# Kernel optimization log

Measured on AMD Instinct MI355X. Metric: run time of the kernel, lower is better.

Reference implementation:

```python
import jax, jax.numpy as jnp
import numpy as np

EMBED_DIM = 512
Q_DIM = 64
V_DIM = 64
WINDOW_SIZE = 128
B, N = 2, 4096


def setup_inputs() -> dict:
    key = jax.random.key(0)
    ks = jax.random.split(key, 7)
    s = 1.0 / np.sqrt(EMBED_DIM)
    u = lambda k, shape: jax.random.uniform(k, shape, jnp.float32, -s, s)
    return {
        "x": jax.random.normal(ks[0], (B, N, EMBED_DIM), jnp.float32),
        "Wq": u(ks[1], (EMBED_DIM, Q_DIM)),
        "bq": u(ks[2], (Q_DIM,)),
        "Wk": u(ks[3], (EMBED_DIM, Q_DIM)),
        "bk": u(ks[4], (Q_DIM,)),
        "Wv": u(ks[5], (EMBED_DIM, V_DIM)),
        "bv": u(ks[6], (V_DIM,)),
    }


def reference(x, Wq, bq, Wk, bk, Wv, bv):
    b, n, _ = x.shape
    w = WINDOW_SIZE // 2
    Q = x @ Wq + bq  # (b, n, Qd)
    K = x @ Wk + bk  # (b, n, Qd)
    V = x @ Wv + bv  # (b, n, Vd)

    diags = jnp.arange(-w, w + 1)            # (nd,) offsets di
    nd = diags.shape[0]
    # Gather K[i + di] via padded K; invalid positions masked to 0 afterwards.
    Kpad = jnp.pad(K, ((0, 0), (w, w), (0, 0)))
    j = jnp.arange(n)[:, None] + diags[None, :]          # (n, nd) = i + di
    Kg = Kpad[:, j + w, :]                               # (b, n, nd, Qd)
    scores = jnp.einsum('bnd,bnod->bno', Q, Kg)          # (b, n, nd)
    valid = (j >= 0) & (j < n)
    scores = jnp.where(valid[None], scores, 0.0)

    # Faithful to original: diagonal dot products are scattered into the FIRST
    # nd columns of a dense (b, n, n) matrix (rest zeros), softmax over the
    # full n columns, then dense matmul with V.
    columns = jnp.zeros((b, n, n), dtype=x.dtype).at[:, :, :nd].set(scores)
    attn = jax.nn.softmax(columns, axis=2)               # (b, n, n)
    return attn @ V                                      # (b, n, Vd)
```

## Files before the change

### kernel.cpp

```cpp
#include <hip/hip_runtime.h>

typedef _Float16 half8 __attribute__((ext_vector_type(8)));
typedef float f32x4 __attribute__((ext_vector_type(4)));

#define NN 4096
#define NE 512
#define HD 64
#define KROWS 4288
#define KOFF  64
#define WSCALE (1.0f / 256.0f)

__device__ __forceinline__ void f16_split(float f, _Float16& hi, _Float16& lo) {
    hi = (_Float16)f;
    lo = (_Float16)(f - (float)hi);
}

#define MFMA16(a, b, c) __builtin_amdgcn_mfma_f32_16x16x32_f16((a), (b), (c), 0, 0, 0)

__global__ __launch_bounds__(256) void wprep_kernel(
    const float* __restrict__ Wq, const float* __restrict__ Wk,
    const float* __restrict__ Wv,
    _Float16* __restrict__ Wf, _Float16* __restrict__ Khi,
    _Float16* __restrict__ Vf, float* __restrict__ Vs)
{
    const int gtid = blockIdx.x * 256 + threadIdx.x;
    const int L = gtid & 63;
    {
        const int nt = (gtid >> 6) % 12;
        const int kt = gtid / 768;
        const int n = nt * 16 + (L & 15);
        const int kbase = kt * 32 + (L >> 4) * 8;
        const float* src; int col;
        if (n < 64)       { src = Wq; col = n; }
        else if (n < 128) { src = Wk; col = n - 64; }
        else              { src = Wv; col = n - 128; }
        half8 sh;
#pragma unroll
        for (int j = 0; j < 8; ++j)
            sh[j] = (_Float16)src[(size_t)(kbase + j) * HD + col];
        *(half8*)(Wf + (size_t)gtid * 8) = sh;
    }
    if (gtid < 6144) {
        const int p = gtid >> 3, o = gtid & 7;
        const int b = p / 192, q = p - b * 192;
        const size_t row = (size_t)b * KROWS + (q < 64 ? q : 4096 + q);
        const half8 z = {0, 0, 0, 0, 0, 0, 0, 0};
        *(half8*)(Khi + row * HD + o * 8) = z;
    }
    if (gtid < 3200) {
        const int rem = gtid % 1600;
        const int jt = rem / 320;
        const int nt = (rem / 64) % 5;
        half8 sh = {0, 0, 0, 0, 0, 0, 0, 0};
        if (nt == 4 && (L & 15) == 0) {
#pragma unroll
            for (int jj = 0; jj < 8; ++jj) {
                const int j = jt * 32 + (L >> 4) * 8 + jj;
                if (j < 129) sh[jj] = (_Float16)1.0f;
            }
        }
        *(half8*)(Vf + (size_t)gtid * 8) = sh;
    }
    if (gtid < 128) Vs[gtid] = 0.f;
}

__global__ __launch_bounds__(1024, 4) void proj_kernel(
    const float* __restrict__ x, const _Float16* __restrict__ Wf,
    const float* __restrict__ bq, const float* __restrict__ bk,
    const float* __restrict__ bv,
    _Float16* __restrict__ Qhi, _Float16* __restrict__ Qlo,
    _Float16* __restrict__ Khi, _Float16* __restrict__ Vf,
    float* __restrict__ Vs)
{
    __shared__ float parts[2][4][3][64][4];
    __shared__ float V_lds[32][68];
    const int tid = threadIdx.x;
    const int L = tid & 63;
    const int w = tid >> 6;
    const int m = L & 15, kg = L >> 4;
    const int blk = blockIdx.x;
    const int b = blk >> 7;
    const int mt = w >> 3;
    const int t3 = (w >> 1) & 3;
    const int h = w & 1;
    const int r0 = blk * 32;
    const int rr = r0 + mt * 16;

    const float* xp = x + (size_t)(rr + m) * NE + h * 256 + kg * 8;
    const _Float16* wfb = Wf + ((size_t)(h * 8) * 12 + t3 * 3) * 512 + L * 8;

    f32x4 acc[3];
#pragma unroll
    for (int t = 0; t < 3; ++t) acc[t] = (f32x4){0.f, 0.f, 0.f, 0.f};

#pragma unroll
    for (int kt = 0; kt < 8; ++kt) {
        const float4 x0 = *(const float4*)(xp + kt * 32);
        const float4 x1 = *(const float4*)(xp + kt * 32 + 4);
        const float xv[8] = {x0.x, x0.y, x0.z, x0.w, x1.x, x1.y, x1.z, x1.w};
        half8 ahi, alo;
#pragma unroll
        for (int j = 0; j < 8; ++j) {
            _Float16 hh, ll; f16_split(xv[j], hh, ll);
            ahi[j] = hh; alo[j] = ll;
        }
#pragma unroll
        for (int t = 0; t < 3; ++t) {
            const half8 wv = *(const half8*)(wfb + (size_t)kt * 6144 + t * 512);
            acc[t] = MFMA16(ahi, wv, acc[t]);
            acc[t] = MFMA16(alo, wv, acc[t]);
        }
    }

    if (h == 1) {
#pragma unroll
        for (int t = 0; t < 3; ++t)
            *(f32x4*)(&parts[mt][t3][t][L][0]) = acc[t];
    }
    __syncthreads();

    if (h == 0) {
#pragma unroll
        for (int t = 0; t < 3; ++t) {
            const f32x4 p = *(const f32x4*)(&parts[mt][t3][t][L][0]);
            acc[t] += p;
            const int nt = t3 * 3 + t;
            const int cgc = nt * 16 + m;
            const float bias = (cgc < 64) ? bq[cgc]
                             : (cgc < 128) ? bk[cgc - 64] : bv[cgc - 128];
#pragma unroll
            for (int r = 0; r < 4; ++r) {
                const int gr = rr + kg * 4 + r;
                const float val = acc[t][r] + bias;
                if (cgc < 64) {
                    _Float16 hh, ll; f16_split(val, hh, ll);
                    Qhi[(size_t)gr * HD + cgc] = hh;
                    Qlo[(size_t)gr * HD + cgc] = ll;
                } else if (cgc < 128) {
                    const int d = cgc - 64, n = gr & 4095;
                    Khi[((size_t)b * KROWS + KOFF + n) * HD + d] = (_Float16)val;
                } else {
                    V_lds[mt * 16 + kg * 4 + r][cgc - 128] = val;
                }
            }
        }
    }
    __syncthreads();

    if (tid < 64) {
        float s = 0.f;
#pragma unroll
        for (int r = 0; r < 32; ++r) s += V_lds[r][tid];
        atomicAdd(&Vs[b * HD + tid], s);
    }

    {
        const int local = blk & 127;
        if (local < 4 && w < 4) {
            const int jt = local;
            const int nt = w;
            half8 sh;
#pragma unroll
            for (int jj = 0; jj < 8; ++jj)
                sh[jj] = (_Float16)V_lds[kg * 8 + jj][nt * 16 + m];
            const size_t fo = ((size_t)((b * 25 + jt * 5 + nt) * 64 + L)) * 8;
            *(half8*)(Vf + fo) = sh;
        } else if (local == 4 && w < 4 && kg == 0) {
            const int nt = w;
            half8 sh = {0, 0, 0, 0, 0, 0, 0, 0};
            sh[0] = (_Float16)V_lds[0][nt * 16 + m];
            const size_t fo = ((size_t)((b * 25 + 4 * 5 + nt) * 64 + L)) * 8;
            *(half8*)(Vf + fo) = sh;
        }
    }
}

__global__ __launch_bounds__(256) void attn_kernel(
    const _Float16* __restrict__ Qhi, const _Float16* __restrict__ Qlo,
    const _Float16* __restrict__ Khi, const _Float16* __restrict__ Vf,
    const float* __restrict__ Vs, float* __restrict__ out)
{
    __shared__ __align__(16) _Float16 wt_hi[16 * 168];
    __shared__ __align__(16) _Float16 wt_lo[16 * 168];
    __shared__ float den_lds[16];

    const int tid = threadIdx.x;
    const int L = tid & 63;
    const int w = tid >> 6;
    const int m = L & 15, kg = L >> 4;
    const int b = blockIdx.x >> 8;
    const int n0 = (blockIdx.x & 255) * 16;

    const float vs = Vs[b * HD + w * 16 + m];

    const _Float16* qp  = Qhi + ((size_t)(b * NN + n0 + m)) * HD + kg * 8;
    const _Float16* qp2 = Qlo + ((size_t)(b * NN + n0 + m)) * HD + kg * 8;
    const half8 qhi0 = *(const half8*)(qp);
    const half8 qhi1 = *(const half8*)(qp + 32);
    const half8 qlo0 = *(const half8*)(qp2);
    const half8 qlo1 = *(const half8*)(qp2 + 32);

    int kts[3]; int nkt;
    if (w == 3) { kts[0] = 3; kts[1] = 7; kts[2] = 8; nkt = 3; }
    else        { kts[0] = w; kts[1] = w + 4; kts[2] = 0; nkt = 2; }

    const _Float16* KB = Khi + (size_t)b * KROWS * HD;
    half8 kh0[3], kh1[3];
#pragma unroll
    for (int i = 0; i < 3; ++i) {
        if (i < nkt) {
            const _Float16* kp = KB + (size_t)(n0 + kts[i] * 16 + m) * HD + kg * 8;
            kh0[i] = *(const half8*)(kp);
            kh1[i] = *(const half8*)(kp + 32);
        }
    }

    half8 vhi[5], vh4[5];
#pragma unroll
    for (int jt = 0; jt < 5; ++jt) {
        const size_t fo = ((size_t)((b * 25 + jt * 5 + w) * 64 + L)) * 8;
        vhi[jt] = *(const half8*)(Vf + fo);
    }
    if (w == 0) {
#pragma unroll
        for (int jt = 0; jt < 5; ++jt) {
            const size_t fo4 = ((size_t)((b * 25 + jt * 5 + 4) * 64 + L)) * 8;
            vh4[jt] = *(const half8*)(Vf + fo4);
        }
    }

    for (int t = tid; t < 1248; t += 256) {
        const int bufsel = t >= 624;
        const int idx = bufsel ? t - 624 : t;
        const int q = idx / 39;
        const int j = 129 + (idx - q * 39);
        (bufsel ? wt_lo : wt_hi)[q * 168 + j] = (_Float16)0.f;
    }

#pragma unroll
    for (int i = 0; i < 3; ++i) {
        if (i < nkt) {
            f32x4 acc = (f32x4){0.f, 0.f, 0.f, 0.f};
            acc = MFMA16(qhi0, kh0[i], acc);
            acc = MFMA16(qhi1, kh1[i], acc);
            acc = MFMA16(qlo0, kh0[i], acc);
            acc = MFMA16(qlo1, kh1[i], acc);
            const int l = kts[i] * 16 + m;
#pragma unroll
            for (int r = 0; r < 4; ++r) {
                const int q = kg * 4 + r;
                const int j = l - q;
                if (j >= 0 && j < 129) {
                    const float wval = (__expf(acc[r]) - 1.0f) * WSCALE;
                    _Float16 hh, ll; f16_split(wval, hh, ll);
                    wt_hi[q * 168 + j] = hh;
                    wt_lo[q * 168 + j] = ll;
                }
            }
        }
    }
    __syncthreads();

    f32x4 oacc = (f32x4){0.f, 0.f, 0.f, 0.f};
    f32x4 dacc = (f32x4){0.f, 0.f, 0.f, 0.f};
#pragma unroll
    for (int jt = 0; jt < 5; ++jt) {
        const half8 whi = *(const half8*)(wt_hi + m * 168 + jt * 32 + kg * 8);
        const half8 wlo = *(const half8*)(wt_lo + m * 168 + jt * 32 + kg * 8);
        oacc = MFMA16(whi, vhi[jt], oacc);
        oacc = MFMA16(wlo, vhi[jt], oacc);
        if (w == 0) {
            dacc = MFMA16(whi, vh4[jt], dacc);
            dacc = MFMA16(wlo, vh4[jt], dacc);
        }
    }
    if (w == 0 && m == 0) {
#pragma unroll
        for (int r = 0; r < 4; ++r) den_lds[kg * 4 + r] = dacc[r];
    }
    __syncthreads();

    {
#pragma unroll
        for (int r = 0; r < 4; ++r) {
            const int q = kg * 4 + r;
            const float val = (vs + 256.0f * oacc[r])
                            / (4096.f + 256.0f * den_lds[q]);
            out[((size_t)(b * NN + n0 + q)) * HD + w * 16 + m] = val;
        }
    }
}

extern "C" void kernel_launch(void* const* d_in, const int* in_sizes, int n_in,
                              void* d_out, int out_size, void* d_ws, size_t ws_size,
                              hipStream_t stream)
{
    const float* x  = (const float*)d_in[0];
    const float* Wq = (const float*)d_in[1];
    const float* bq = (const float*)d_in[2];
    const float* Wk = (const float*)d_in[3];
    const float* bk = (const float*)d_in[4];
    const float* Wv = (const float*)d_in[5];
    const float* bv = (const float*)d_in[6];
    float* out = (float*)d_out;

    char* ws = (char*)d_ws;
    float*     Vs  = (float*)(ws + 0);
    _Float16*  Khi = (_Float16*)(ws + 512);
    _Float16*  Qhi = (_Float16*)(ws + 1098240);
    _Float16*  Qlo = (_Float16*)(ws + 2146816);
    _Float16*  Wf  = (_Float16*)(ws + 3195392);
    _Float16*  Vf  = (_Float16*)(ws + 3392000);

    wprep_kernel<<<48, 256, 0, stream>>>(Wq, Wk, Wv, Wf, Khi, Vf, Vs);
    proj_kernel<<<256, 1024, 0, stream>>>(x, Wf, bq, bk, bv,
                                          Qhi, Qlo, Khi, Vf, Vs);
    attn_kernel<<<512, 256, 0, stream>>>(Qhi, Qlo, Khi, Vf, Vs, out);
}
```

Measured before the change: 95.63 us.

## Process 32 query rows per attention block with 8 waves; spread weight prep over more blocks

The attention kernel now handles 32 query rows per block using 512 threads (8 waves) instead of 16 rows with 4 waves, so the grid halves to 256 blocks. Score tiles are redistributed across waves by query-tile and key-tile, and two waves compute the softmax denominators. The weight prep kernel switches from 48 blocks of 256 threads to 192 blocks of 64 threads to spread its work across more CUs. The larger tile lets overlapping K tiles be shared within a block, at the cost of fewer blocks on the device and a larger LDS footprint per block.

```diff
diff --git a/kernel.cpp b/kernel.cpp
--- a/kernel.cpp
+++ b/kernel.cpp
@@ -17,13 +17,13 @@
 
 #define MFMA16(a, b, c) __builtin_amdgcn_mfma_f32_16x16x32_f16((a), (b), (c), 0, 0, 0)
 
-__global__ __launch_bounds__(256) void wprep_kernel(
+__global__ __launch_bounds__(64) void wprep_kernel(
     const float* __restrict__ Wq, const float* __restrict__ Wk,
     const float* __restrict__ Wv,
     _Float16* __restrict__ Wf, _Float16* __restrict__ Khi,
     _Float16* __restrict__ Vf, float* __restrict__ Vs)
 {
-    const int gtid = blockIdx.x * 256 + threadIdx.x;
+    const int gtid = blockIdx.x * 64 + threadIdx.x;
     const int L = gtid & 63;
     {
         const int nt = (gtid >> 6) % 12;
@@ -175,34 +175,40 @@
     }
 }
 
-__global__ __launch_bounds__(256) void attn_kernel(
+__global__ __launch_bounds__(512) void attn_kernel(
     const _Float16* __restrict__ Qhi, const _Float16* __restrict__ Qlo,
     const _Float16* __restrict__ Khi, const _Float16* __restrict__ Vf,
     const float* __restrict__ Vs, float* __restrict__ out)
 {
-    __shared__ __align__(16) _Float16 wt_hi[16 * 168];
-    __shared__ __align__(16) _Float16 wt_lo[16 * 168];
-    __shared__ float den_lds[16];
+    __shared__ __align__(16) _Float16 wt_hi[32 * 168];
+    __shared__ __align__(16) _Float16 wt_lo[32 * 168];
+    __shared__ float den_lds[32];
 
     const int tid = threadIdx.x;
     const int L = tid & 63;
     const int w = tid >> 6;
     const int m = L & 15, kg = L >> 4;
-    const int b = blockIdx.x >> 8;
-    const int n0 = (blockIdx.x & 255) * 16;
-
-    const float vs = Vs[b * HD + w * 16 + m];
-
-    const _Float16* qp  = Qhi + ((size_t)(b * NN + n0 + m)) * HD + kg * 8;
-    const _Float16* qp2 = Qlo + ((size_t)(b * NN + n0 + m)) * HD + kg * 8;
+    const int b = blockIdx.x >> 7;
+    const int n0 = (blockIdx.x & 127) * 32;
+    const int qt = w & 1;
+    const int mt = w >> 2;
+    const int nt = w & 3;
+    const bool den_wave = (w == 0) || (w == 6);
+
+    const float vs = Vs[b * HD + nt * 16 + m];
+
+    const _Float16* qp  = Qhi + ((size_t)(b * NN + n0 + qt * 16 + m)) * HD + kg * 8;
+    const _Float16* qp2 = Qlo + ((size_t)(b * NN + n0 + qt * 16 + m)) * HD + kg * 8;
     const half8 qhi0 = *(const half8*)(qp);
     const half8 qhi1 = *(const half8*)(qp + 32);
     const half8 qlo0 = *(const half8*)(qp2);
     const half8 qlo1 = *(const half8*)(qp2 + 32);
 
+    const int i4 = w >> 1;
+    const int f = (i4 == 0) ? 1 : (i4 == 1) ? 2 : (i4 == 2) ? 0 : 3;
     int kts[3]; int nkt;
-    if (w == 3) { kts[0] = 3; kts[1] = 7; kts[2] = 8; nkt = 3; }
-    else        { kts[0] = w; kts[1] = w + 4; kts[2] = 0; nkt = 2; }
+    kts[0] = f + qt; kts[1] = f + qt + 4; kts[2] = f + qt + 8;
+    nkt = (i4 == 2) ? 3 : 2;
 
     const _Float16* KB = Khi + (size_t)b * KROWS * HD;
     half8 kh0[3], kh1[3];
@@ -218,10 +224,10 @@
     half8 vhi[5], vh4[5];
 #pragma unroll
     for (int jt = 0; jt < 5; ++jt) {
-        const size_t fo = ((size_t)((b * 25 + jt * 5 + w) * 64 + L)) * 8;
+        const size_t fo = ((size_t)((b * 25 + jt * 5 + nt) * 64 + L)) * 8;
         vhi[jt] = *(const half8*)(Vf + fo);
     }
-    if (w == 0) {
+    if (den_wave) {
 #pragma unroll
         for (int jt = 0; jt < 5; ++jt) {
             const size_t fo4 = ((size_t)((b * 25 + jt * 5 + 4) * 64 + L)) * 8;
@@ -229,11 +235,11 @@
         }
     }
 
-    for (int t = tid; t < 1248; t += 256) {
-        const int bufsel = t >= 624;
-        const int idx = bufsel ? t - 624 : t;
-        const int q = idx / 39;
-        const int j = 129 + (idx - q * 39);
+    for (int t = tid; t < 2048; t += 512) {
+        const int bufsel = t >= 1024;
+        const int idx = t & 1023;
+        const int q = idx >> 5;
+        const int j = 129 + (idx & 31);
         (bufsel ? wt_lo : wt_hi)[q * 168 + j] = (_Float16)0.f;
     }
 
@@ -248,7 +254,7 @@
             const int l = kts[i] * 16 + m;
 #pragma unroll
             for (int r = 0; r < 4; ++r) {
-                const int q = kg * 4 + r;
+                const int q = qt * 16 + kg * 4 + r;
                 const int j = l - q;
                 if (j >= 0 && j < 129) {
                     const float wval = (__expf(acc[r]) - 1.0f) * WSCALE;
@@ -265,28 +271,28 @@
     f32x4 dacc = (f32x4){0.f, 0.f, 0.f, 0.f};
 #pragma unroll
     for (int jt = 0; jt < 5; ++jt) {
-        const half8 whi = *(const half8*)(wt_hi + m * 168 + jt * 32 + kg * 8);
-        const half8 wlo = *(const half8*)(wt_lo + m * 168 + jt * 32 + kg * 8);
+        const half8 whi = *(const half8*)(wt_hi + (mt * 16 + m) * 168 + jt * 32 + kg * 8);
+        const half8 wlo = *(const half8*)(wt_lo + (mt * 16 + m) * 168 + jt * 32 + kg * 8);
         oacc = MFMA16(whi, vhi[jt], oacc);
         oacc = MFMA16(wlo, vhi[jt], oacc);
-        if (w == 0) {
+        if (den_wave) {
             dacc = MFMA16(whi, vh4[jt], dacc);
             dacc = MFMA16(wlo, vh4[jt], dacc);
         }
     }
-    if (w == 0 && m == 0) {
-#pragma unroll
-        for (int r = 0; r < 4; ++r) den_lds[kg * 4 + r] = dacc[r];
+    if (den_wave && m == 0) {
+#pragma unroll
+        for (int r = 0; r < 4; ++r) den_lds[mt * 16 + kg * 4 + r] = dacc[r];
     }
     __syncthreads();
 
     {
 #pragma unroll
         for (int r = 0; r < 4; ++r) {
-            const int q = kg * 4 + r;
+            const int q = mt * 16 + kg * 4 + r;
             const float val = (vs + 256.0f * oacc[r])
                             / (4096.f + 256.0f * den_lds[q]);
-            out[((size_t)(b * NN + n0 + q)) * HD + w * 16 + m] = val;
+            out[((size_t)(b * NN + n0 + q)) * HD + nt * 16 + m] = val;
         }
     }
 }
@@ -312,8 +318,8 @@
     _Float16*  Wf  = (_Float16*)(ws + 3195392);
     _Float16*  Vf  = (_Float16*)(ws + 3392000);
 
-    wprep_kernel<<<48, 256, 0, stream>>>(Wq, Wk, Wv, Wf, Khi, Vf, Vs);
+    wprep_kernel<<<192, 64, 0, stream>>>(Wq, Wk, Wv, Wf, Khi, Vf, Vs);
     proj_kernel<<<256, 1024, 0, stream>>>(x, Wf, bq, bk, bv,
                                           Qhi, Qlo, Khi, Vf, Vs);
-    attn_kernel<<<512, 256, 0, stream>>>(Qhi, Qlo, Khi, Vf, Vs, out);
-}
+    attn_kernel<<<256, 512, 0, stream>>>(Qhi, Qlo, Khi, Vf, Vs, out);
+}
```

Result: no change. 94.76 us (-0.9%).
